# Kernel optimization log

Measured on AMD Instinct MI355X. Metric: run time of the kernel, lower is better.

## Reference

```python
import jax, jax.numpy as jnp
import numpy as np

HEAD_SIZE = 64
N_EMBD = 1024

def setup_inputs() -> dict:
    key = jax.random.key(0)
    ks = jax.random.split(key, 7)
    B, T = 4, 4096
    s = 1.0 / np.sqrt(N_EMBD)
    return {
        "x": jax.random.normal(ks[0], (B, T, N_EMBD), dtype=jnp.float32),
        "Wq": jax.random.normal(ks[1], (N_EMBD, HEAD_SIZE), dtype=jnp.float32) * s,
        "bq": jnp.zeros((HEAD_SIZE,), dtype=jnp.float32),
        "Wk": jax.random.normal(ks[2], (N_EMBD, HEAD_SIZE), dtype=jnp.float32) * s,
        "bk": jnp.zeros((HEAD_SIZE,), dtype=jnp.float32),
        "Wv": jax.random.normal(ks[3], (N_EMBD, HEAD_SIZE), dtype=jnp.float32) * s,
        "bv": jnp.zeros((HEAD_SIZE,), dtype=jnp.float32),
    }

def reference(x, Wq, bq, Wk, bk, Wv, bv):
    # q,k,v: [B,T,H]
    q = x @ Wq + bq
    k = x @ Wk + bk
    v = x @ Wv + bv
    scale = jnp.asarray(HEAD_SIZE, x.dtype) ** -0.5
    att = jnp.einsum("bth,bsh->bts", q, k) * scale  # [B,T,T]
    att = jax.nn.softmax(att, axis=-1)
    # dropout with p=0.0 is identity (eval-mode reference)
    return jnp.einsum("bts,bsh->bth", att, v)
```

## Files before the change

kernel.cpp:

```cpp
#include <hip/hip_runtime.h>
#include <hip/hip_bf16.h>
#include <cmath>

#define BATCH 4
#define TLEN  4096
#define CEMB  1024
#define HEAD  64
#define NROWS (BATCH * TLEN)

typedef __bf16 bf16;
typedef __attribute__((ext_vector_type(8))) __bf16 bf16x8;
typedef __attribute__((ext_vector_type(4))) __bf16 bf16x4;
typedef __attribute__((ext_vector_type(4))) float f32x4;

#define QSCALE 0.1803368801111204f

static __device__ __forceinline__ f32x4 mfma16(bf16x8 a, bf16x8 b, f32x4 c) {
    return __builtin_amdgcn_mfma_f32_16x16x32_bf16(a, b, c, 0, 0, 0);
}

static __device__ __forceinline__ void async_ld16(const void* g, void* l) {
    __builtin_amdgcn_global_load_lds(
        (const __attribute__((address_space(1))) void*)g,
        (__attribute__((address_space(3))) void*)l, 16, 0, 0);
}

__global__ __launch_bounds__(256) void pack_w(
    const float* __restrict__ Wq, const float* __restrict__ Wk,
    const float* __restrict__ Wv, bf16* __restrict__ Wt)
{
    const int n = blockIdx.x;
    const int which = n >> 6, h = n & 63;
    const float* W = which == 0 ? Wq : (which == 1 ? Wk : Wv);
    const float s = which == 0 ? QSCALE : 1.0f;
    for (int k = threadIdx.x; k < CEMB; k += 256)
        Wt[(size_t)n * CEMB + k] = (bf16)(W[(size_t)k * HEAD + h] * s);
}

__global__ __launch_bounds__(256, 2) void qkv(
    const float* __restrict__ x, const bf16* __restrict__ Wt,
    const float* __restrict__ bq, const float* __restrict__ bk,
    const float* __restrict__ bv,
    bf16* __restrict__ qb, bf16* __restrict__ kb, bf16* __restrict__ vT)
{
    __shared__ __align__(16) float Xsh[2][2][32][64];

    const int tid  = threadIdx.x;
    const int lane = tid & 63;
    const int wvid = tid >> 6;
    const int quad = lane >> 4;
    const int col  = lane & 15;
    const int row0 = blockIdx.x * 32;

    const float* xblk = x + (size_t)row0 * CEMB;
    const bf16* wrow[3];
    #pragma unroll
    for (int j = 0; j < 3; ++j)
        wrow[j] = Wt + (size_t)((wvid * 3 + j) * 16 + col) * CEMB + quad * 8;

    const int sr = lane >> 4;
    const int ss = lane & 15;
    auto stage = [&](int ci, int bufi) {
        #pragma unroll
        for (int h2 = 0; h2 < 2; ++h2)
            #pragma unroll
            for (int j = 0; j < 2; ++j) {
                const int r = wvid * 8 + j * 4 + sr;
                const int c = ss ^ (r & 7);
                async_ld16(xblk + (size_t)r * CEMB + ci * 128 + h2 * 64 + c * 4,
                           &Xsh[bufi][h2][wvid * 8 + j * 4][0]);
            }
    };

    f32x4 acc[2][3] = {};
    const int c7 = col & 7;

    stage(0, 0);
    int buf = 0;
    for (int ci = 0; ci < 8; ++ci) {
        __syncthreads();
        if (ci + 1 < 8) stage(ci + 1, buf ^ 1);

        #pragma unroll
        for (int kk = 0; kk < 4; ++kk) {
            const int h  = ci * 4 + kk;
            const int hf = kk >> 1;
            const int kl = kk & 1;
            bf16x8 Bv[3];
            #pragma unroll
            for (int j = 0; j < 3; ++j)
                Bv[j] = *(const bf16x8*)(wrow[j] + h * 32);
            #pragma unroll
            for (int rt = 0; rt < 2; ++rt) {
                const int r = rt * 16 + col;
                const int g0 = kl * 8 + quad * 2;
                float4 a0 = *(const float4*)&Xsh[buf][hf][r][(g0 ^ c7) * 4];
                float4 a1 = *(const float4*)&Xsh[buf][hf][r][((g0 + 1) ^ c7) * 4];
                bf16x8 af;
                af[0]=(bf16)a0.x; af[1]=(bf16)a0.y; af[2]=(bf16)a0.z; af[3]=(bf16)a0.w;
                af[4]=(bf16)a1.x; af[5]=(bf16)a1.y; af[6]=(bf16)a1.z; af[7]=(bf16)a1.w;
                #pragma unroll
                for (int j = 0; j < 3; ++j)
                    acc[rt][j] = mfma16(af, Bv[j], acc[rt][j]);
            }
        }
        buf ^= 1;
    }

    const float* bias[3] = {bq, bk, bv};
    #pragma unroll
    for (int j = 0; j < 3; ++j) {
        const int jg = wvid * 3 + j;
        const int which = jg >> 2;
        const int h = (jg & 3) * 16 + col;
        float bb = bias[which][h];
        if (which == 0) bb *= QSCALE;
        #pragma unroll
        for (int rt = 0; rt < 2; ++rt) {
            if (which < 2) {
                bf16* dst = which == 0 ? qb : kb;
                #pragma unroll
                for (int r = 0; r < 4; ++r) {
                    const int trow = row0 + rt * 16 + quad * 4 + r;
                    dst[(size_t)trow * HEAD + h] = (bf16)(acc[rt][j][r] + bb);
                }
            } else {
                bf16x4 pv;
                #pragma unroll
                for (int r = 0; r < 4; ++r) pv[r] = (bf16)(acc[rt][j][r] + bb);
                const int trow0 = row0 + rt * 16 + quad * 4;
                const int bb_   = trow0 >> 12;
                const int tt    = trow0 & (TLEN - 1);
                *(bf16x4*)(vT + ((size_t)(bb_ * HEAD + h)) * TLEN + tt) = pv;
            }
        }
    }
}

__global__ __launch_bounds__(256, 2) void attn(
    const bf16* __restrict__ qb, const bf16* __restrict__ kb,
    const bf16* __restrict__ vT,
    bf16* __restrict__ opart, float* __restrict__ lpart,
    float* __restrict__ out, int nsplit, int lg2S)
{
    __shared__ __align__(16) bf16 Ksh[2][64][64];
    __shared__ __align__(16) bf16 Vsh[2][64][64];
    __shared__ __align__(16) bf16 Psh[4][16][64];

    const int tid  = threadIdx.x;
    const int lane = tid & 63;
    const int wvid = tid >> 6;
    const int quad = lane >> 4;
    const int col  = lane & 15;

    int b, sp, qtile;
    {
        const int id = blockIdx.x;
        if (nsplit >= 2) {
            const int cpx = (BATCH << lg2S) >> 3;
            const int idx = id >> 3;
            const int combo = (id & 7) * cpx + (idx >> 4);
            qtile = idx & 15;
            b = combo >> lg2S;
            sp = combo & (nsplit - 1);
        } else {
            qtile = id & 15; b = id >> 4; sp = 0;
        }
    }
    const int q0 = qtile * 256 + wvid * 64;
    const size_t rowbase = (size_t)b * TLEN + q0;

    bf16x8 qf[4][2];
    #pragma unroll
    for (int qt = 0; qt < 4; ++qt) {
        const bf16* qp = qb + (rowbase + qt * 16 + col) * HEAD + quad * 8;
        qf[qt][0] = *(const bf16x8*)qp;
        qf[qt][1] = *(const bf16x8*)(qp + 32);
    }
    const bf16* kbB = kb + (size_t)b * TLEN * HEAD;
    const bf16* vTB = vT + (size_t)b * HEAD * TLEN;

    f32x4 o[4][4] = {};
    float lsum[4] = {0.f, 0.f, 0.f, 0.f};

    const int slen = TLEN >> lg2S;
    const int sbeg = sp * slen;
    const int nch  = slen / 64;

    const int r8 = lane >> 3;
    const int s8 = lane & 7;
    auto stage = [&](int s0, int bufi) {
        #pragma unroll
        for (int j = 0; j < 2; ++j) {
            const int r = wvid * 16 + j * 8 + r8;
            const int c = s8 ^ (r & 7);
            async_ld16(kbB + (size_t)(s0 + r) * HEAD + c * 8,
                       &Ksh[bufi][wvid * 16 + j * 8][0]);
            async_ld16(vTB + (size_t)r * TLEN + s0 + c * 8,
                       &Vsh[bufi][wvid * 16 + j * 8][0]);
        }
    };

    stage(sbeg, 0);
    int buf = 0;
    for (int ci = 0; ci < nch; ++ci) {
        __syncthreads();
        if (ci + 1 < nch) stage(sbeg + (ci + 1) * 64, buf ^ 1);

        const int c7 = col & 7;
        bf16x8 kf[4][2];
        #pragma unroll
        for (int t = 0; t < 4; ++t) {
            const int r = t * 16 + col;
            kf[t][0] = *(const bf16x8*)&Ksh[buf][r][(quad ^ c7) * 8];
            kf[t][1] = *(const bf16x8*)&Ksh[buf][r][((4 + quad) ^ c7) * 8];
        }
        bf16x8 pb[4][2];
        bf16* Pb = &Psh[wvid][col][0];
        #pragma unroll
        for (int qt = 0; qt < 4; ++qt) {
            f32x4 st[4];
            #pragma unroll
            for (int t = 0; t < 4; ++t) {
                f32x4 z = {0.f, 0.f, 0.f, 0.f};
                z = mfma16(kf[t][0], qf[qt][0], z);
                z = mfma16(kf[t][1], qf[qt][1], z);
                st[t] = z;
            }
            #pragma unroll
            for (int t = 0; t < 4; ++t) {
                float p0 = __builtin_amdgcn_exp2f(st[t][0]);
                float p1 = __builtin_amdgcn_exp2f(st[t][1]);
                float p2 = __builtin_amdgcn_exp2f(st[t][2]);
                float p3 = __builtin_amdgcn_exp2f(st[t][3]);
                lsum[qt] += (p0 + p1) + (p2 + p3);
                bf16x4 pv = {(bf16)p0, (bf16)p1, (bf16)p2, (bf16)p3};
                const int g = ((2 * t + (quad >> 1)) ^ c7) * 8 + (quad & 1) * 4;
                *(bf16x4*)(Pb + g) = pv;
            }
            pb[qt][0] = *(const bf16x8*)(Pb + ((quad ^ c7) * 8));
            pb[qt][1] = *(const bf16x8*)(Pb + (((4 + quad) ^ c7) * 8));
        }
        #pragma unroll
        for (int ht = 0; ht < 4; ++ht) {
            const int r = ht * 16 + col;
            bf16x8 v0 = *(const bf16x8*)&Vsh[buf][r][(quad ^ c7) * 8];
            bf16x8 v1 = *(const bf16x8*)&Vsh[buf][r][((4 + quad) ^ c7) * 8];
            #pragma unroll
            for (int qt = 0; qt < 4; ++qt) {
                o[qt][ht] = mfma16(v0, pb[qt][0], o[qt][ht]);
                o[qt][ht] = mfma16(v1, pb[qt][1], o[qt][ht]);
            }
        }
        buf ^= 1;
    }

    #pragma unroll
    for (int qt = 0; qt < 4; ++qt) {
        lsum[qt] += __shfl_xor(lsum[qt], 16, 64);
        lsum[qt] += __shfl_xor(lsum[qt], 32, 64);
    }

    #pragma unroll
    for (int qt = 0; qt < 4; ++qt) {
        const size_t grow = rowbase + qt * 16 + col;
        if (nsplit == 1) {
            const float inv = 1.f / lsum[qt];
            float* ob = out + grow * HEAD;
            #pragma unroll
            for (int ht = 0; ht < 4; ++ht) {
                f32x4 r = o[qt][ht] * inv;
                *(f32x4*)(ob + ht * 16 + quad * 4) = r;
            }
        } else if (sp == 0) {
            float* ob = out + grow * HEAD;
            #pragma unroll
            for (int ht = 0; ht < 4; ++ht)
                *(f32x4*)(ob + ht * 16 + quad * 4) = o[qt][ht];
            if (quad == 0) lpart[grow] = lsum[qt];
        } else {
            bf16* ob = opart + ((size_t)(sp - 1) * NROWS + grow) * HEAD;
            #pragma unroll
            for (int ht = 0; ht < 4; ++ht) {
                bf16x4 r;
                #pragma unroll
                for (int rr = 0; rr < 4; ++rr) r[rr] = (bf16)o[qt][ht][rr];
                *(bf16x4*)(ob + ht * 16 + quad * 4) = r;
            }
            if (quad == 0) lpart[(size_t)sp * NROWS + grow] = lsum[qt];
        }
    }
}

__global__ __launch_bounds__(256) void combine(
    const bf16* __restrict__ opart, const float* __restrict__ lpart,
    float* __restrict__ out, int nsplit)
{
    const int gid = blockIdx.x * 256 + threadIdx.x;
    const int row = gid >> 4;
    const int h4  = (gid & 15) * 4;

    float L = 0.f;
    for (int s = 0; s < nsplit; ++s) L += lpart[(size_t)s * NROWS + row];
    f32x4 O = *(const f32x4*)(out + (size_t)row * HEAD + h4);
    for (int s = 1; s < nsplit; ++s) {
        bf16x4 v = *(const bf16x4*)(opart + ((size_t)(s - 1) * NROWS + row) * HEAD + h4);
        O[0] += (float)v[0]; O[1] += (float)v[1];
        O[2] += (float)v[2]; O[3] += (float)v[3];
    }
    f32x4 r = O * (1.f / L);
    *(f32x4*)(out + (size_t)row * HEAD + h4) = r;
}

extern "C" void kernel_launch(void* const* d_in, const int* in_sizes, int n_in,
                              void* d_out, int out_size, void* d_ws, size_t ws_size,
                              hipStream_t stream) {
    const float* x  = (const float*)d_in[0];
    const float* Wq = (const float*)d_in[1];
    const float* bq = (const float*)d_in[2];
    const float* Wk = (const float*)d_in[3];
    const float* bk = (const float*)d_in[4];
    const float* Wv = (const float*)d_in[5];
    const float* bv = (const float*)d_in[6];
    float* out = (float*)d_out;

    const size_t n_tok = (size_t)NROWS * HEAD;
    char* ws = (char*)d_ws;
    bf16* qb = (bf16*)ws;
    bf16* kb = qb + n_tok;
    bf16* vT = kb + n_tok;
    bf16* Wt = vT + n_tok;
    const size_t base = 3 * n_tok * sizeof(bf16) + 192 * CEMB * sizeof(bf16);

    auto need = [&](int S) {
        return base + (size_t)(S - 1) * n_tok * sizeof(bf16)
                    + (size_t)S * NROWS * sizeof(float);
    };
    int S = 1, lg2S = 0;
    if      (ws_size >= need(8)) { S = 8; lg2S = 3; }
    else if (ws_size >= need(4)) { S = 4; lg2S = 2; }
    else if (ws_size >= need(2)) { S = 2; lg2S = 1; }
    bf16*  opart = Wt + 192 * CEMB;
    float* lpart = (float*)(opart + (size_t)(S - 1) * n_tok);

    pack_w<<<dim3(192), dim3(256), 0, stream>>>(Wq, Wk, Wv, Wt);
    qkv<<<dim3(512), dim3(256), 0, stream>>>(x, Wt, bq, bk, bv, qb, kb, vT);
    attn<<<dim3(16 * BATCH * S), dim3(256), 0, stream>>>(
        qb, kb, vT, opart, lpart, out, S, lg2S);
    if (S > 1)
        combine<<<dim3((NROWS * 16) / 256), dim3(256), 0, stream>>>(
            opart, lpart, out, S);
}
```

Before: 160.5 us.

## Switch attention to 32x32x16 MFMA and pass P through permlane32 swaps

Rewrites the attention inner loop to use 32x32x16 bf16 MFMA tiles instead of 16x16x32. The score-to-probability transform now packs exp2 results with v_cvt_pk_bf16 and rearranges them into B-operand layout with permlane32_swap, replacing the round trip through the per-wave Psh shared-memory buffer. This removes LDS writes and reads plus shuffle steps and frees LDS, at the cost of larger accumulator register footprints (f32x16) that may pressure registers at 2 waves/SIMD occupancy.

```diff
diff --git a/kernel.cpp b/kernel.cpp
--- a/kernel.cpp
+++ b/kernel.cpp
@@ -12,11 +12,21 @@
 typedef __attribute__((ext_vector_type(8))) __bf16 bf16x8;
 typedef __attribute__((ext_vector_type(4))) __bf16 bf16x4;
 typedef __attribute__((ext_vector_type(4))) float f32x4;
+typedef __attribute__((ext_vector_type(16))) float f32x16;
+typedef __attribute__((ext_vector_type(4))) unsigned u32x4;
 
 #define QSCALE 0.1803368801111204f
 
 static __device__ __forceinline__ f32x4 mfma16(bf16x8 a, bf16x8 b, f32x4 c) {
     return __builtin_amdgcn_mfma_f32_16x16x32_bf16(a, b, c, 0, 0, 0);
+}
+static __device__ __forceinline__ f32x16 mfma32(bf16x8 a, bf16x8 b, f32x16 c) {
+    return __builtin_amdgcn_mfma_f32_32x32x16_bf16(a, b, c, 0, 0, 0);
+}
+static __device__ __forceinline__ unsigned cvt_pk_bf16(float lo, float hi) {
+    unsigned r;
+    asm("v_cvt_pk_bf16_f32 %0, %1, %2" : "=v"(r) : "v"(lo), "v"(hi));
+    return r;
 }
 
 static __device__ __forceinline__ void async_ld16(const void* g, void* l) {
@@ -145,13 +155,12 @@
 {
     __shared__ __align__(16) bf16 Ksh[2][64][64];
     __shared__ __align__(16) bf16 Vsh[2][64][64];
-    __shared__ __align__(16) bf16 Psh[4][16][64];
 
     const int tid  = threadIdx.x;
     const int lane = tid & 63;
     const int wvid = tid >> 6;
-    const int quad = lane >> 4;
-    const int col  = lane & 15;
+    const int l31  = lane & 31;
+    const int b5   = lane >> 5;
 
     int b, sp, qtile;
     {
@@ -170,18 +179,19 @@
     const int q0 = qtile * 256 + wvid * 64;
     const size_t rowbase = (size_t)b * TLEN + q0;
 
-    bf16x8 qf[4][2];
-    #pragma unroll
-    for (int qt = 0; qt < 4; ++qt) {
-        const bf16* qp = qb + (rowbase + qt * 16 + col) * HEAD + quad * 8;
-        qf[qt][0] = *(const bf16x8*)qp;
-        qf[qt][1] = *(const bf16x8*)(qp + 32);
-    }
+    bf16x8 qf[2][4];
+    #pragma unroll
+    for (int qt = 0; qt < 2; ++qt)
+        #pragma unroll
+        for (int m = 0; m < 4; ++m)
+            qf[qt][m] = *(const bf16x8*)
+                (qb + (rowbase + qt * 32 + l31) * HEAD + m * 16 + b5 * 8);
+
     const bf16* kbB = kb + (size_t)b * TLEN * HEAD;
     const bf16* vTB = vT + (size_t)b * HEAD * TLEN;
 
-    f32x4 o[4][4] = {};
-    float lsum[4] = {0.f, 0.f, 0.f, 0.f};
+    f32x16 o[2][2] = {};
+    float lsum[2] = {0.f, 0.f};
 
     const int slen = TLEN >> lg2S;
     const int sbeg = sp * slen;
@@ -207,87 +217,103 @@
         __syncthreads();
         if (ci + 1 < nch) stage(sbeg + (ci + 1) * 64, buf ^ 1);
 
-        const int c7 = col & 7;
-        bf16x8 kf[4][2];
-        #pragma unroll
-        for (int t = 0; t < 4; ++t) {
-            const int r = t * 16 + col;
-            kf[t][0] = *(const bf16x8*)&Ksh[buf][r][(quad ^ c7) * 8];
-            kf[t][1] = *(const bf16x8*)&Ksh[buf][r][((4 + quad) ^ c7) * 8];
-        }
-        bf16x8 pb[4][2];
-        bf16* Pb = &Psh[wvid][col][0];
-        #pragma unroll
-        for (int qt = 0; qt < 4; ++qt) {
-            f32x4 st[4];
-            #pragma unroll
-            for (int t = 0; t < 4; ++t) {
-                f32x4 z = {0.f, 0.f, 0.f, 0.f};
-                z = mfma16(kf[t][0], qf[qt][0], z);
-                z = mfma16(kf[t][1], qf[qt][1], z);
-                st[t] = z;
-            }
-            #pragma unroll
-            for (int t = 0; t < 4; ++t) {
-                float p0 = __builtin_amdgcn_exp2f(st[t][0]);
-                float p1 = __builtin_amdgcn_exp2f(st[t][1]);
-                float p2 = __builtin_amdgcn_exp2f(st[t][2]);
-                float p3 = __builtin_amdgcn_exp2f(st[t][3]);
-                lsum[qt] += (p0 + p1) + (p2 + p3);
-                bf16x4 pv = {(bf16)p0, (bf16)p1, (bf16)p2, (bf16)p3};
-                const int g = ((2 * t + (quad >> 1)) ^ c7) * 8 + (quad & 1) * 4;
-                *(bf16x4*)(Pb + g) = pv;
-            }
-            pb[qt][0] = *(const bf16x8*)(Pb + ((quad ^ c7) * 8));
-            pb[qt][1] = *(const bf16x8*)(Pb + (((4 + quad) ^ c7) * 8));
-        }
-        #pragma unroll
-        for (int ht = 0; ht < 4; ++ht) {
-            const int r = ht * 16 + col;
-            bf16x8 v0 = *(const bf16x8*)&Vsh[buf][r][(quad ^ c7) * 8];
-            bf16x8 v1 = *(const bf16x8*)&Vsh[buf][r][((4 + quad) ^ c7) * 8];
-            #pragma unroll
-            for (int qt = 0; qt < 4; ++qt) {
-                o[qt][ht] = mfma16(v0, pb[qt][0], o[qt][ht]);
-                o[qt][ht] = mfma16(v1, pb[qt][1], o[qt][ht]);
+        #pragma unroll
+        for (int kt = 0; kt < 2; ++kt) {
+            const int kr = kt * 32 + l31;
+            const int k7 = kr & 7;
+            bf16x8 kf[4];
+            #pragma unroll
+            for (int m = 0; m < 4; ++m)
+                kf[m] = *(const bf16x8*)&Ksh[buf][kr][((2 * m + b5) ^ k7) * 8];
+
+            bf16x8 pb[2][2];
+            #pragma unroll
+            for (int qt = 0; qt < 2; ++qt) {
+                f32x16 st = {};
+                #pragma unroll
+                for (int m = 0; m < 4; ++m)
+                    st = mfma32(kf[m], qf[qt][m], st);
+                float e[16];
+                #pragma unroll
+                for (int r = 0; r < 16; ++r)
+                    e[r] = __builtin_amdgcn_exp2f(st[r]);
+                float t0 = (e[0] + e[1]) + (e[2] + e[3]);
+                float t1 = (e[4] + e[5]) + (e[6] + e[7]);
+                float t2 = (e[8] + e[9]) + (e[10] + e[11]);
+                float t3 = (e[12] + e[13]) + (e[14] + e[15]);
+                lsum[qt] += (t0 + t1) + (t2 + t3);
+                unsigned w[8];
+                #pragma unroll
+                for (int s = 0; s < 8; ++s)
+                    w[s] = cvt_pk_bf16(e[2 * s], e[2 * s + 1]);
+                #pragma unroll
+                for (int kc = 0; kc < 2; ++kc) {
+                    auto s02 = __builtin_amdgcn_permlane32_swap(
+                        w[4 * kc + 0], w[4 * kc + 2], false, false);
+                    auto s13 = __builtin_amdgcn_permlane32_swap(
+                        w[4 * kc + 1], w[4 * kc + 3], false, false);
+                    u32x4 pw = { (unsigned)s02[0], (unsigned)s13[0],
+                                 (unsigned)s02[1], (unsigned)s13[1] };
+                    pb[qt][kc] = __builtin_bit_cast(bf16x8, pw);
+                }
+            }
+            #pragma unroll
+            for (int ht = 0; ht < 2; ++ht) {
+                const int vr = ht * 32 + l31;
+                const int v7 = vr & 7;
+                #pragma unroll
+                for (int kc = 0; kc < 2; ++kc) {
+                    bf16x8 vf = *(const bf16x8*)
+                        &Vsh[buf][vr][((2 * (2 * kt + kc) + b5) ^ v7) * 8];
+                    #pragma unroll
+                    for (int qt = 0; qt < 2; ++qt)
+                        o[qt][ht] = mfma32(vf, pb[qt][kc], o[qt][ht]);
+                }
             }
         }
         buf ^= 1;
     }
 
     #pragma unroll
-    for (int qt = 0; qt < 4; ++qt) {
-        lsum[qt] += __shfl_xor(lsum[qt], 16, 64);
+    for (int qt = 0; qt < 2; ++qt)
         lsum[qt] += __shfl_xor(lsum[qt], 32, 64);
-    }
-
-    #pragma unroll
-    for (int qt = 0; qt < 4; ++qt) {
-        const size_t grow = rowbase + qt * 16 + col;
+
+    #pragma unroll
+    for (int qt = 0; qt < 2; ++qt) {
+        const size_t grow = rowbase + qt * 32 + l31;
         if (nsplit == 1) {
             const float inv = 1.f / lsum[qt];
             float* ob = out + grow * HEAD;
             #pragma unroll
-            for (int ht = 0; ht < 4; ++ht) {
-                f32x4 r = o[qt][ht] * inv;
-                *(f32x4*)(ob + ht * 16 + quad * 4) = r;
-            }
+            for (int ht = 0; ht < 2; ++ht)
+                #pragma unroll
+                for (int g = 0; g < 4; ++g) {
+                    f32x4 r = { o[qt][ht][4*g+0] * inv, o[qt][ht][4*g+1] * inv,
+                                o[qt][ht][4*g+2] * inv, o[qt][ht][4*g+3] * inv };
+                    *(f32x4*)(ob + ht * 32 + g * 8 + b5 * 4) = r;
+                }
         } else if (sp == 0) {
             float* ob = out + grow * HEAD;
             #pragma unroll
-            for (int ht = 0; ht < 4; ++ht)
-                *(f32x4*)(ob + ht * 16 + quad * 4) = o[qt][ht];
-            if (quad == 0) lpart[grow] = lsum[qt];
+            for (int ht = 0; ht < 2; ++ht)
+                #pragma unroll
+                for (int g = 0; g < 4; ++g) {
+                    f32x4 r = { o[qt][ht][4*g+0], o[qt][ht][4*g+1],
+                                o[qt][ht][4*g+2], o[qt][ht][4*g+3] };
+                    *(f32x4*)(ob + ht * 32 + g * 8 + b5 * 4) = r;
+                }
+            if (lane < 32) lpart[grow] = lsum[qt];
         } else {
             bf16* ob = opart + ((size_t)(sp - 1) * NROWS + grow) * HEAD;
             #pragma unroll
-            for (int ht = 0; ht < 4; ++ht) {
-                bf16x4 r;
-                #pragma unroll
-                for (int rr = 0; rr < 4; ++rr) r[rr] = (bf16)o[qt][ht][rr];
-                *(bf16x4*)(ob + ht * 16 + quad * 4) = r;
-            }
-            if (quad == 0) lpart[(size_t)sp * NROWS + grow] = lsum[qt];
+            for (int ht = 0; ht < 2; ++ht)
+                #pragma unroll
+                for (int g = 0; g < 4; ++g) {
+                    bf16x4 r = { (bf16)o[qt][ht][4*g+0], (bf16)o[qt][ht][4*g+1],
+                                 (bf16)o[qt][ht][4*g+2], (bf16)o[qt][ht][4*g+3] };
+                    *(bf16x4*)(ob + ht * 32 + g * 8 + b5 * 4) = r;
+                }
+            if (lane < 32) lpart[(size_t)sp * NROWS + grow] = lsum[qt];
         }
     }
 }
```

Result: no change. 159.2 us (-0.8%).
